# Optimization experiments

Measured on AMD Instinct MI355X. Metric: run time of the kernel, lower is better.

Reference implementation:

```python
import jax, jax.numpy as jnp
import numpy as np

N_NODE = 200001   # n_user + n_item + 1
N_USER = 100000
N_ITEM = 100000
K = 4
D = 64
NCONVS = 2
NT = 64000        # nodes in the batched graph
E = 400000        # edges in the batched graph
B = 128
L = 50
MAX_TIME = 1000.0
MIN_TIME = 0.0


def setup_inputs() -> dict:
    key = jax.random.key(0)
    ks = jax.random.split(key, 16)
    embed = jax.random.normal(ks[0], (N_NODE, K, D), jnp.float32) * 0.1
    delta = jnp.ones((N_USER,), jnp.float32)
    tau_p = jnp.ones((N_ITEM,), jnp.float32)
    W1 = jax.random.normal(ks[1], (D, D), jnp.float32) * 0.1
    W2 = jax.random.normal(ks[2], (D, D), jnp.float32) * 0.1
    uid = jax.random.randint(ks[3], (B,), 0, N_USER)
    sid = jax.random.randint(ks[4], (B,), 0, N_ITEM)
    node_ids = jax.random.randint(ks[5], (NT,), 0, N_NODE)
    edge_index = jax.random.randint(ks[6], (2, E), 0, NT)
    seq_map = jax.random.randint(ks[7], (B, L), 0, NT)
    tar_map = jax.random.randint(ks[8], (B,), 0, NT)
    seq_idx = jax.random.randint(ks[9], (B, L), 0, N_ITEM)
    seq_len = jax.random.randint(ks[10], (B,), 1, L + 1)
    seqs_time = jax.random.uniform(ks[11], (B, L), jnp.float32) * (MAX_TIME - MIN_TIME) + MIN_TIME
    clk_time = jax.random.uniform(ks[12], (B,), jnp.float32) * (MAX_TIME - MIN_TIME) + MIN_TIME
    return dict(embed=embed, delta=delta, tau_p=tau_p, W1=W1, W2=W2,
                seqs_time=seqs_time, clk_time=clk_time,
                uid=uid, sid=sid, node_ids=node_ids, edge_index=edge_index,
                seq_map=seq_map, tar_map=tar_map, seq_idx=seq_idx, seq_len=seq_len)


def _cos(a, b):
    # torch.cosine_similarity with eps=1e-8 clamp on each norm
    na = jnp.maximum(jnp.sqrt((a * a).sum(-1)), 1e-8)
    nb = jnp.maximum(jnp.sqrt((b * b).sum(-1)), 1e-8)
    return (a * b).sum(-1) / (na * nb)


def reference(embed, delta, tau_p, W1, W2, seqs_time, clk_time,
              uid, sid, node_ids, edge_index, seq_map, tar_map, seq_idx, seq_len):
    row, col = edge_index[0], edge_index[1]
    x = embed[node_ids]                                    # [NT, K, D]

    # symmetric degree normalization (degree of target nodes, as in PyG degree(col))
    deg = jax.ops.segment_sum(jnp.ones((E,), x.dtype), col, num_segments=NT)
    dinv = jnp.where(deg > 0, deg ** -0.5, 0.0)
    base = dinv[row] * dinv[col]                           # [E]

    s = jnp.ones((K, E), x.dtype)
    for _ in range(NCONVS):
        s_q = jax.nn.softmax(s, axis=0)                    # [K, E] channel routing
        w = (base[None, :] * s_q).T                        # [E, K]
        msg = x[row] * w[:, :, None]                       # [E, K, D]
        x = jax.ops.segment_sum(msg, col, num_segments=NT) # aggr='add'
        z = (x[row] * jnp.tanh(x[col])).sum(-1)            # [E, K] tanh-gated edge score
        s = s + z.T

    resi = embed[node_ids[seq_map]]                        # [B, L, K, D] residual (pre-conv embeds)
    seq_embed = jnp.einsum('blkd,ed->blke', x[seq_map], W1) + resi
    mask = jnp.arange(L)[None, :] < seq_len[:, None]       # [B, L]
    seq_embed = jnp.where(mask[:, :, None, None], seq_embed, 0.0)  # pad_sequence(0)

    a_v = jnp.einsum('bkd,ed->bke', x[tar_map], W2) + embed[sid + N_USER]  # [B, K, D]
    a_u = embed[uid]                                                       # [B, K, D]

    mu_u_v = _cos(a_u, a_v)                                # [B, K]
    gamma_h_v = _cos(seq_embed, a_v[:, None])              # [B, L, K]
    j = jnp.exp(-(clk_time[:, None] - seqs_time) / (MAX_TIME - MIN_TIME) * delta[uid][:, None])
    j = jnp.where(mask, j, 0.0)                            # [B, L]

    logits = _cos(seq_embed, a_u[:, None])                 # [B, L, K]
    eps = 1e-4
    u_k = jax.random.uniform(jax.random.key(1), logits.shape, jnp.float32,
                             minval=eps, maxval=1.0 - eps)
    g_k = -jnp.log(-jnp.log(u_k))                          # Gumbel noise
    pi = jax.nn.softmax((logits + g_k) / tau_p[seq_idx][:, :, None], axis=-1)

    inc = j[:, :, None] * gamma_h_v * pi                   # [B, L, K]
    return (mu_u_v + inc.sum(1)).mean(-1)                  # [B]
```

## Files before the change

### kernel.cpp

```cpp
#include <hip/hip_runtime.h>
#include <math.h>

#define NT_     64000
#define E_      400000
#define B_      128
#define L_      50
#define KD_     256
#define D_      64
#define N_USER_ 100000
#define MAXN_   (B_*L_ + B_)
#define CAP_    48

__device__ __forceinline__ float wred(float v){
#pragma unroll
  for(int s=32;s;s>>=1) v += __shfl_xor(v, s, 64);
  return v;
}

__device__ __forceinline__ unsigned rotl(unsigned x, int r){ return (x<<r)|(x>>(32-r)); }

__device__ void tf2x32(unsigned c0, unsigned c1, unsigned &o0, unsigned &o1){
  const unsigned k0=0u, k1=1u;
  const unsigned k2=k0^k1^0x1BD11BDAu;
  unsigned x0=c0+k0, x1=c1+k1;
  const int RA[4]={13,15,26,6};
  const int RB[4]={17,29,16,24};
#pragma unroll
  for(int i=0;i<4;i++){ x0+=x1; x1=rotl(x1,RA[i]); x1^=x0; }
  x0+=k1; x1+=k2+1u;
#pragma unroll
  for(int i=0;i<4;i++){ x0+=x1; x1=rotl(x1,RB[i]); x1^=x0; }
  x0+=k2; x1+=k0+2u;
#pragma unroll
  for(int i=0;i<4;i++){ x0+=x1; x1=rotl(x1,RA[i]); x1^=x0; }
  x0+=k0; x1+=k1+3u;
#pragma unroll
  for(int i=0;i<4;i++){ x0+=x1; x1=rotl(x1,RB[i]); x1^=x0; }
  x0+=k1; x1+=k2+4u;
#pragma unroll
  for(int i=0;i<4;i++){ x0+=x1; x1=rotl(x1,RA[i]); x1^=x0; }
  x0+=k2; x1+=k0+5u;
  o0=x0; o1=x1;
}

__device__ float gumbel_at(int idx){
  unsigned o0,o1;
  tf2x32(0u, (unsigned)idx, o0, o1);
  unsigned bits = o0 ^ o1;
  unsigned fb = (bits>>9) | 0x3f800000u;
  float f = __uint_as_float(fb) - 1.0f;
  const float mn=1e-4f, mx=1.0f-1e-4f;
  float u = fmaxf(mn, f*(mx-mn)+mn);
  return -logf(-logf(u));
}

__global__ void fill_all(const int* __restrict__ seq_map, const int* __restrict__ tar_map,
                         const int* __restrict__ row, const int* __restrict__ col,
                         const int* __restrict__ node_ids,
                         int* __restrict__ markpos, int* __restrict__ nlist,
                         int* __restrict__ ncount, int* __restrict__ need,
                         int* __restrict__ cnt, int2* __restrict__ pk2){
  int i = blockIdx.x*256 + threadIdx.x;
  if(i < MAXN_){
    int n = (i < B_*L_) ? seq_map[i] : tar_map[i - B_*L_];
    int old = atomicCAS(&markpos[n], 0, -1);
    if(old == 0){
      int s = atomicAdd(ncount, 1);
      nlist[s] = n;
      need[n] = 1;
      markpos[n] = s + 1;
    }
  }
  if(i < E_){
    int c = col[i], r = row[i];
    int j = atomicAdd(&cnt[c], 1);
    if(j < CAP_) pk2[c*CAP_ + j] = make_int2(node_ids[r], r);
  }
}

__global__ void dinv_need(const int* __restrict__ cnt, const int2* __restrict__ pk2,
                          const int* __restrict__ nlist, const int* __restrict__ ncount,
                          const float* __restrict__ W1, const float* __restrict__ W2,
                          float* __restrict__ dinv, int* __restrict__ need,
                          float* __restrict__ W1T, float* __restrict__ W2T){
  int b = blockIdx.x, t = threadIdx.x;
  if(b < NT_/256){
    int i = b*256 + t;
    int v = cnt[i];
    dinv[i] = (v>0) ? (1.0f/sqrtf((float)v)) : 0.0f;
  } else if(b < NT_/256 + (MAXN_+255)/256){
    int s = (b - NT_/256)*256 + t;
    if(s < *ncount){
      int c = nlist[s];
      int d = cnt[c]; if(d > CAP_) d = CAP_;
      int base = c*CAP_;
      for(int j=0;j<d;j++) need[pk2[base+j].y] = 1;
    }
  } else {
    int tb = b - (NT_/256 + (MAXN_+255)/256);
    int idx = (tb & 15)*256 + t;
    int e = idx >> 6, d = idx & 63;
    if(tb < 16) W1T[d*64 + e] = W1[e*64 + d];
    else        W2T[d*64 + e] = W2[e*64 + d];
  }
}

__global__ void aggregate1(const float4* __restrict__ embed4, const int* __restrict__ cnt,
                           const int2* __restrict__ pk2, const float* __restrict__ dinv,
                           const int* __restrict__ need, float4* __restrict__ x14){
  int wv = threadIdx.x>>6, lane = threadIdx.x&63;
  int c = blockIdx.x*4 + wv;
  if(!need[c]) return;
  int deg = cnt[c]; if(deg > CAP_) deg = CAP_;
  int base = c*CAP_;
  float dc = dinv[c]*0.25f;
  float4 acc = {0.f,0.f,0.f,0.f};
  for(int i=0; i<deg; i+=8){
    int idx[8]; float w[8];
#pragma unroll
    for(int j=0;j<8;j++){
      bool ok = (i+j) < deg;
      int2 pr = pk2[ok ? (base+i+j) : base];
      idx[j] = pr.x;
      w[j]   = ok ? dinv[pr.y]*dc : 0.f;
    }
#pragma unroll
    for(int j=0;j<8;j++){
      float4 v = embed4[(size_t)idx[j]*64 + lane];
      acc.x = fmaf(v.x, w[j], acc.x);
      acc.y = fmaf(v.y, w[j], acc.y);
      acc.z = fmaf(v.z, w[j], acc.z);
      acc.w = fmaf(v.w, w[j], acc.w);
    }
  }
  x14[(size_t)c*64+lane] = acc;
}

__global__ void conv2_fused(const float* __restrict__ x1, const int* __restrict__ cnt,
                            const int2* __restrict__ pk2, const float* __restrict__ dinv,
                            const int* __restrict__ nlist, const int* __restrict__ ncount,
                            float* __restrict__ x2c){
  int slot = blockIdx.x;
  if(slot >= *ncount) return;
  int c = nlist[slot];
  int t = threadIdx.x, k = t>>6, lane = t&63;
  float tx = tanhf(x1[(size_t)c*KD_ + t]);
  float acc = 0.f;
  __shared__ float zs[4];
  int deg = cnt[c]; if(deg > CAP_) deg = CAP_;
  int base = c*CAP_;
  float dc4 = 4.f*dinv[c]*0.25f;
  for(int i=0;i<deg;i++){
    int2 rec = pk2[base+i];
    int r = rec.y;
    float xr = x1[(size_t)r*KD_ + t];
    float zk = wred(xr*tx);
    if(lane==0) zs[k] = zk;
    __syncthreads();
    float z0=zs[0], z1=zs[1], z2=zs[2], z3=zs[3];
    float m = fmaxf(fmaxf(z0,z1), fmaxf(z2,z3));
    float e0=expf(z0-m), e1=expf(z1-m), e2=expf(z2-m), e3=expf(z3-m);
    float inv = (dinv[r]*dc4)/(e0+e1+e2+e3);
    float w = ((k==0)?e0:(k==1)?e1:(k==2)?e2:e3) * inv;
    acc = fmaf(xr, w, acc);
    __syncthreads();
  }
  x2c[(size_t)slot*KD_ + t] = acc;
}

__global__ void head_fused(const float* __restrict__ embed, const float* __restrict__ x2c,
                           const int* __restrict__ markpos,
                           const float* __restrict__ W1T, const float* __restrict__ W2T,
                           const int* __restrict__ node_ids, const int* __restrict__ seq_map,
                           const int* __restrict__ tar_map, const int* __restrict__ seq_idx,
                           const int* __restrict__ seq_len,
                           const int* __restrict__ uid, const int* __restrict__ sid,
                           const float* __restrict__ seqs_time, const float* __restrict__ clk_time,
                           const float* __restrict__ tau_p, const float* __restrict__ delta,
                           float* __restrict__ mu, float* __restrict__ acc){
  int bl = blockIdx.x;
  int b = bl / L_, l = bl % L_;
  if(l >= seq_len[b]) return;
  int t = threadIdx.x, k = t>>6, lane = t&63;
  __shared__ float sxt[KD_], sxv[KD_];
  int n = seq_map[bl];
  sxt[t] = x2c[(size_t)(markpos[tar_map[b]]-1)*KD_ + t];
  sxv[t] = x2c[(size_t)(markpos[n]-1)*KD_ + t];
  __syncthreads();
  float av = embed[((size_t)(N_USER_ + sid[b]))*KD_ + t];
  float se = embed[(size_t)node_ids[n]*KD_ + t];
  const float* xt_k = sxt + k*64;
  const float* xv_k = sxv + k*64;
#pragma unroll 8
  for(int d=0; d<64; d++){
    av = fmaf(xt_k[d], W2T[d*64 + lane], av);
    se = fmaf(xv_k[d], W1T[d*64 + lane], se);
  }
  float au = embed[(size_t)uid[b]*KD_ + t];
  float nv  = wred(av*av);
  float nu  = wred(au*au);
  float duv = wred(av*au);
  float dv  = wred(se*av);
  float du  = wred(se*au);
  float ns  = wred(se*se);
  __shared__ float s6[6][4];
  if(lane==0){ s6[0][k]=nv; s6[1][k]=nu; s6[2][k]=duv; s6[3][k]=dv; s6[4][k]=du; s6[5][k]=ns; }
  __syncthreads();
  if(t==0){
    float jv  = expf(-(clk_time[b]-seqs_time[bl]) * (1.0f/1000.0f) * delta[uid[b]]);
    float tau = tau_p[seq_idx[bl]];
    float gam[4], lg[4];
    float m = -1e30f;
#pragma unroll
    for(int kk=0;kk<4;kk++){
      float rnv = fmaxf(sqrtf(s6[0][kk]), 1e-8f);
      float rnu = fmaxf(sqrtf(s6[1][kk]), 1e-8f);
      float ins = 1.f/fmaxf(sqrtf(s6[5][kk]), 1e-8f);
      if(l==0) mu[b*4+kk] = s6[2][kk]/(rnv*rnu);
      gam[kk] = s6[3][kk]*ins/rnv;
      float logit = s6[4][kk]*ins/rnu;
      lg[kk] = (logit + gumbel_at(bl*4+kk))/tau;
      m = fmaxf(m, lg[kk]);
    }
    float es[4], ssum=0.f;
#pragma unroll
    for(int kk=0;kk<4;kk++){ es[kk]=expf(lg[kk]-m); ssum+=es[kk]; }
    float isum = 1.f/ssum;
#pragma unroll
    for(int kk=0;kk<4;kk++)
      atomicAdd(&acc[b*4+kk], jv * gam[kk] * es[kk]*isum);
  }
}

__global__ void finalize(const float* __restrict__ mu, const float* __restrict__ acc,
                         float* __restrict__ out){
  int b = threadIdx.x;
  if(b < B_){
    float s = 0.f;
#pragma unroll
    for(int k=0;k<4;k++) s += mu[b*4+k] + acc[b*4+k];
    out[b] = s * 0.25f;
  }
}

extern "C" void kernel_launch(void* const* d_in, const int* in_sizes, int n_in,
                              void* d_out, int out_size, void* d_ws, size_t ws_size,
                              hipStream_t stream){
  const float* embed = (const float*)d_in[0];
  const float* delta = (const float*)d_in[1];
  const float* tau_p = (const float*)d_in[2];
  const float* W1    = (const float*)d_in[3];
  const float* W2    = (const float*)d_in[4];
  const float* seqs_time = (const float*)d_in[5];
  const float* clk_time  = (const float*)d_in[6];
  const int* uid      = (const int*)d_in[7];
  const int* sid      = (const int*)d_in[8];
  const int* node_ids = (const int*)d_in[9];
  const int* edge_index = (const int*)d_in[10];
  const int* seq_map  = (const int*)d_in[11];
  const int* tar_map  = (const int*)d_in[12];
  const int* seq_idx  = (const int*)d_in[13];
  const int* seq_len  = (const int*)d_in[14];
  const int* row = edge_index;
  const int* col = edge_index + E_;
  float* out = (float*)d_out;

  char* wp = (char*)d_ws;
  size_t o = 0;
  auto carve = [&](size_t bytes)->char*{ char* r = wp + o; o = (o + bytes + 255) & ~(size_t)255; return r; };
  float* acc     = (float*)carve((size_t)B_*4*4);
  int*   ncount  = (int*)  carve((size_t)4);
  int*   cnt     = (int*)  carve((size_t)NT_*4);
  int*   need    = (int*)  carve((size_t)NT_*4);
  int*   markpos = (int*)  carve((size_t)NT_*4);
  char*  zero_end = wp + o;
  float* mu      = (float*)carve((size_t)B_*4*4);
  int*   nlist   = (int*)  carve((size_t)MAXN_*4);
  float* dinv    = (float*)carve((size_t)NT_*4);
  float* W1T     = (float*)carve((size_t)64*64*4);
  float* W2T     = (float*)carve((size_t)64*64*4);
  int2*  pk2     = (int2*) carve((size_t)NT_*CAP_*8);
  float* x2c     = (float*)carve((size_t)MAXN_*KD_*4);
  float* x1      = (float*)carve((size_t)NT_*KD_*4);

  hipMemsetAsync(acc, 0, (size_t)(zero_end - (char*)acc), stream);

  fill_all<<<(E_+255)/256, 256, 0, stream>>>(seq_map, tar_map, row, col, node_ids,
                                             markpos, nlist, ncount, need, cnt, pk2);
  dinv_need<<<NT_/256 + (MAXN_+255)/256 + 32, 256, 0, stream>>>(cnt, pk2, nlist, ncount,
                                                                W1, W2, dinv, need, W1T, W2T);
  aggregate1<<<NT_/4, 256, 0, stream>>>((const float4*)embed, cnt, pk2, dinv,
                                        need, (float4*)x1);
  conv2_fused<<<MAXN_, 256, 0, stream>>>(x1, cnt, pk2, dinv, nlist, ncount, x2c);
  head_fused<<<B_*L_, 256, 0, stream>>>(embed, x2c, markpos, W1T, W2T,
                                        node_ids, seq_map, tar_map, seq_idx, seq_len,
                                        uid, sid, seqs_time, clk_time, tau_p, delta,
                                        mu, acc);
  finalize<<<1, 128, 0, stream>>>(mu, acc, out);
}
```

Before: 159.1 us.

## Precompute per-edge normalization weights and batch conv2 neighbor reductions by eight

The dinv array is replaced by per-edge weights (dinv[row]*dinv[col]*0.25), computed once in the prep kernel and read directly by aggregate1 and conv2. This removes the dependent dinv[r] gather from both inner loops. conv2_fused now handles neighbors in groups of eight, doing all wave reductions before a single pair of barriers, where it previously synchronized twice per edge. The cost is an extra NT*CAP float buffer and more serial per-thread work in prep. Per-row dinv is now recomputed from cnt inside the weight loop.

```diff
diff --git a/kernel.cpp b/kernel.cpp
--- a/kernel.cpp
+++ b/kernel.cpp
@@ -78,51 +78,60 @@
   }
 }
 
-__global__ void dinv_need(const int* __restrict__ cnt, const int2* __restrict__ pk2,
-                          const int* __restrict__ nlist, const int* __restrict__ ncount,
-                          const float* __restrict__ W1, const float* __restrict__ W2,
-                          float* __restrict__ dinv, int* __restrict__ need,
-                          float* __restrict__ W1T, float* __restrict__ W2T){
+__global__ void prep_all(const int* __restrict__ cnt, const int2* __restrict__ pk2,
+                         const int* __restrict__ nlist, const int* __restrict__ ncount,
+                         const float* __restrict__ W1, const float* __restrict__ W2,
+                         int* __restrict__ need, float* __restrict__ W1T,
+                         float* __restrict__ W2T, float* __restrict__ wgt){
+  const int NB_NEED = (MAXN_+255)/256;
   int b = blockIdx.x, t = threadIdx.x;
-  if(b < NT_/256){
-    int i = b*256 + t;
-    int v = cnt[i];
-    dinv[i] = (v>0) ? (1.0f/sqrtf((float)v)) : 0.0f;
-  } else if(b < NT_/256 + (MAXN_+255)/256){
-    int s = (b - NT_/256)*256 + t;
+  if(b < NB_NEED){
+    int s = b*256 + t;
     if(s < *ncount){
       int c = nlist[s];
       int d = cnt[c]; if(d > CAP_) d = CAP_;
       int base = c*CAP_;
       for(int j=0;j<d;j++) need[pk2[base+j].y] = 1;
     }
-  } else {
-    int tb = b - (NT_/256 + (MAXN_+255)/256);
+  } else if(b < NB_NEED + 32){
+    int tb = b - NB_NEED;
     int idx = (tb & 15)*256 + t;
     int e = idx >> 6, d = idx & 63;
     if(tb < 16) W1T[d*64 + e] = W1[e*64 + d];
     else        W2T[d*64 + e] = W2[e*64 + d];
+  } else {
+    int c = (b - NB_NEED - 32)*256 + t;
+    int d = cnt[c]; if(d > CAP_) d = CAP_;
+    if(d > 0){
+      float dc = (1.0f/sqrtf((float)cnt[c]))*0.25f;
+      int base = c*CAP_;
+      for(int j=0;j<d;j++){
+        int r = pk2[base+j].y;
+        int cr = cnt[r];
+        float dr = (cr>0) ? (1.0f/sqrtf((float)cr)) : 0.0f;
+        wgt[base+j] = dr*dc;
+      }
+    }
   }
 }
 
 __global__ void aggregate1(const float4* __restrict__ embed4, const int* __restrict__ cnt,
-                           const int2* __restrict__ pk2, const float* __restrict__ dinv,
+                           const int2* __restrict__ pk2, const float* __restrict__ wgt,
                            const int* __restrict__ need, float4* __restrict__ x14){
   int wv = threadIdx.x>>6, lane = threadIdx.x&63;
   int c = blockIdx.x*4 + wv;
   if(!need[c]) return;
   int deg = cnt[c]; if(deg > CAP_) deg = CAP_;
   int base = c*CAP_;
-  float dc = dinv[c]*0.25f;
   float4 acc = {0.f,0.f,0.f,0.f};
   for(int i=0; i<deg; i+=8){
     int idx[8]; float w[8];
 #pragma unroll
     for(int j=0;j<8;j++){
       bool ok = (i+j) < deg;
-      int2 pr = pk2[ok ? (base+i+j) : base];
-      idx[j] = pr.x;
-      w[j]   = ok ? dinv[pr.y]*dc : 0.f;
+      int s = ok ? (base+i+j) : base;
+      idx[j] = pk2[s].x;
+      w[j]   = ok ? wgt[s] : 0.f;
     }
 #pragma unroll
     for(int j=0;j<8;j++){
@@ -137,7 +146,7 @@
 }
 
 __global__ void conv2_fused(const float* __restrict__ x1, const int* __restrict__ cnt,
-                            const int2* __restrict__ pk2, const float* __restrict__ dinv,
+                            const int2* __restrict__ pk2, const float* __restrict__ wgt,
                             const int* __restrict__ nlist, const int* __restrict__ ncount,
                             float* __restrict__ x2c){
   int slot = blockIdx.x;
@@ -146,23 +155,27 @@
   int t = threadIdx.x, k = t>>6, lane = t&63;
   float tx = tanhf(x1[(size_t)c*KD_ + t]);
   float acc = 0.f;
-  __shared__ float zs[4];
+  __shared__ float zs[8][4];
   int deg = cnt[c]; if(deg > CAP_) deg = CAP_;
   int base = c*CAP_;
-  float dc4 = 4.f*dinv[c]*0.25f;
-  for(int i=0;i<deg;i++){
-    int2 rec = pk2[base+i];
-    int r = rec.y;
-    float xr = x1[(size_t)r*KD_ + t];
-    float zk = wred(xr*tx);
-    if(lane==0) zs[k] = zk;
+  for(int i0=0; i0<deg; i0+=8){
+    int nb = deg - i0; nb = (nb>8)?8:nb;
+    float xr8[8];
+    for(int j=0;j<nb;j++){
+      int r = pk2[base+i0+j].y;
+      xr8[j] = x1[(size_t)r*KD_ + t];
+      float zk = wred(xr8[j]*tx);
+      if(lane==0) zs[j][k] = zk;
+    }
     __syncthreads();
-    float z0=zs[0], z1=zs[1], z2=zs[2], z3=zs[3];
-    float m = fmaxf(fmaxf(z0,z1), fmaxf(z2,z3));
-    float e0=expf(z0-m), e1=expf(z1-m), e2=expf(z2-m), e3=expf(z3-m);
-    float inv = (dinv[r]*dc4)/(e0+e1+e2+e3);
-    float w = ((k==0)?e0:(k==1)?e1:(k==2)?e2:e3) * inv;
-    acc = fmaf(xr, w, acc);
+    for(int j=0;j<nb;j++){
+      float z0=zs[j][0], z1=zs[j][1], z2=zs[j][2], z3=zs[j][3];
+      float m = fmaxf(fmaxf(z0,z1), fmaxf(z2,z3));
+      float e0=expf(z0-m), e1=expf(z1-m), e2=expf(z2-m), e3=expf(z3-m);
+      float inv = (4.f*wgt[base+i0+j])/(e0+e1+e2+e3);
+      float w = ((k==0)?e0:(k==1)?e1:(k==2)?e2:e3) * inv;
+      acc = fmaf(xr8[j], w, acc);
+    }
     __syncthreads();
   }
   x2c[(size_t)slot*KD_ + t] = acc;
@@ -276,10 +289,10 @@
   char*  zero_end = wp + o;
   float* mu      = (float*)carve((size_t)B_*4*4);
   int*   nlist   = (int*)  carve((size_t)MAXN_*4);
-  float* dinv    = (float*)carve((size_t)NT_*4);
   float* W1T     = (float*)carve((size_t)64*64*4);
   float* W2T     = (float*)carve((size_t)64*64*4);
   int2*  pk2     = (int2*) carve((size_t)NT_*CAP_*8);
+  float* wgt     = (float*)carve((size_t)NT_*CAP_*4);
   float* x2c     = (float*)carve((size_t)MAXN_*KD_*4);
   float* x1      = (float*)carve((size_t)NT_*KD_*4);
 
@@ -287,11 +300,11 @@
 
   fill_all<<<(E_+255)/256, 256, 0, stream>>>(seq_map, tar_map, row, col, node_ids,
                                              markpos, nlist, ncount, need, cnt, pk2);
-  dinv_need<<<NT_/256 + (MAXN_+255)/256 + 32, 256, 0, stream>>>(cnt, pk2, nlist, ncount,
-                                                                W1, W2, dinv, need, W1T, W2T);
-  aggregate1<<<NT_/4, 256, 0, stream>>>((const float4*)embed, cnt, pk2, dinv,
+  prep_all<<<(MAXN_+255)/256 + 32 + NT_/256, 256, 0, stream>>>(cnt, pk2, nlist, ncount,
+                                                               W1, W2, need, W1T, W2T, wgt);
+  aggregate1<<<NT_/4, 256, 0, stream>>>((const float4*)embed, cnt, pk2, wgt,
                                         need, (float4*)x1);
-  conv2_fused<<<MAXN_, 256, 0, stream>>>(x1, cnt, pk2, dinv, nlist, ncount, x2c);
+  conv2_fused<<<MAXN_, 256, 0, stream>>>(x1, cnt, pk2, wgt, nlist, ncount, x2c);
   head_fused<<<B_*L_, 256, 0, stream>>>(embed, x2c, markpos, W1T, W2T,
                                         node_ids, seq_map, tar_map, seq_idx, seq_len,
                                         uid, sid, seqs_time, clk_time, tau_p, delta,
```

Measured after the change: 157.8 us. Within noise of the previous version (-0.9%).
